# Kernel optimization log

Measured on AMD Instinct MI355X. Metric: run time of the kernel, lower is better.

## Reference

```python
import jax, jax.numpy as jnp
import numpy as np

B, C, W = 32768, 142, 10
K, D = 4096, 128
EPS = 1e-5


def _ln(x, g, b):
    m = jnp.mean(x, axis=-1, keepdims=True)
    v = jnp.var(x, axis=-1, keepdims=True)
    return (x - m) * jax.lax.rsqrt(v + EPS) * g + b


def setup_inputs() -> dict:
    key = jax.random.key(0)
    ks = jax.random.split(key, 10)
    s = lambda fi, fo: (2.0 / (fi + fo)) ** 0.5
    return {
        "x": jax.random.normal(ks[0], (B, C, W), jnp.float32),
        "W1": jax.random.normal(ks[1], (1420, 512), jnp.float32) * s(1420, 512),
        "b1": jnp.zeros((512,), jnp.float32),
        "g1": jnp.ones((512,), jnp.float32),
        "be1": jnp.zeros((512,), jnp.float32),
        "W2": jax.random.normal(ks[2], (512, 256), jnp.float32) * s(512, 256),
        "b2": jnp.zeros((256,), jnp.float32),
        "g2": jnp.ones((256,), jnp.float32),
        "be2": jnp.zeros((256,), jnp.float32),
        "W3": jax.random.normal(ks[3], (256, D), jnp.float32) * s(256, D),
        "b3": jnp.zeros((D,), jnp.float32),
        "emb": jax.random.normal(ks[4], (K, D), jnp.float32),
        "W4": jax.random.normal(ks[5], (D, 256), jnp.float32) * s(D, 256),
        "b4": jnp.zeros((256,), jnp.float32),
        "g3": jnp.ones((256,), jnp.float32),
        "be3": jnp.zeros((256,), jnp.float32),
        "W5": jax.random.normal(ks[6], (256, 128), jnp.float32) * s(256, 128),
        "b5": jnp.zeros((128,), jnp.float32),
        "W6": jax.random.normal(ks[7], (128, 2), jnp.float32) * s(128, 2),
        "b6": jnp.zeros((2,), jnp.float32),
    }


def reference(x, W1, b1, g1, be1, W2, b2, g2, be2, W3, b3, emb,
              W4, b4, g3, be3, W5, b5, W6, b6):
    # ----- encoder (eval mode: dropout is identity) -----
    xf = x.reshape(x.shape[0], -1)                      # [B, 1420]
    h = jax.nn.gelu(_ln(xf @ W1 + b1, g1, be1), approximate=False)
    h = jax.nn.gelu(_ln(h @ W2 + b2, g2, be2), approximate=False)
    z_e = h @ W3 + b3                                   # [B, D]

    # ----- EMA VQ (eval: no buffer updates) -----
    # squared distances give the same argmin as torch.cdist
    d2 = (jnp.sum(z_e * z_e, axis=-1, keepdims=True)
          - 2.0 * (z_e @ emb.T)
          + jnp.sum(emb * emb, axis=-1))                # [B, K]
    indices = jnp.argmin(d2, axis=-1)                   # [B] int
    z_q = emb[indices]                                  # [B, D]

    commitment_loss = 0.25 * jnp.mean((jax.lax.stop_gradient(z_q) - z_e) ** 2)
    z_q_st = z_e + jax.lax.stop_gradient(z_q - z_e)     # straight-through

    # histogram instead of materializing [B, K] one-hot
    counts = jnp.zeros((K,), jnp.float32).at[indices].add(1.0)
    avg_probs = counts / x.shape[0]
    perplexity = jnp.exp(-jnp.sum(avg_probs * jnp.log(avg_probs + 1e-10)))
    n_active = jnp.sum(avg_probs > 0.001)

    # ----- decoder (eval mode) -----
    d = jax.nn.gelu(_ln(z_q_st @ W4 + b4, g3, be3), approximate=False)
    d = jax.nn.gelu(d @ W5 + b5, approximate=False)
    velocity_pred = d @ W6 + b6                         # [B, 2]

    return (velocity_pred, z_e, z_q_st, indices, commitment_loss,
            perplexity, n_active)
```

## Files before the change

kernel.cpp:

```cpp
#include <hip/hip_runtime.h>

#define B_ROWS 32768
#define KCODES 4096

typedef float f32x4 __attribute__((ext_vector_type(4)));
typedef _Float16 f16x8 __attribute__((ext_vector_type(8)));
typedef _Float16 f16x4 __attribute__((ext_vector_type(4)));

struct Split { _Float16 h, m; };

__device__ __forceinline__ Split split2(float v)
{
  Split s;
  s.h = (_Float16)v;
  s.m = (_Float16)((v - (float)s.h) * 256.f);
  return s;
}

template<bool SPLITA>
__global__ __launch_bounds__(256, 3)
void hgemm(const float* __restrict__ Af, const _Float16* __restrict__ Ah,
           const _Float16* __restrict__ Am, int Astr,
           const _Float16* __restrict__ Bh, const _Float16* __restrict__ Bm,
           const float* __restrict__ bias, float* __restrict__ C,
           int M, int N, int K, int Kp, int nbx)
{
  __shared__ _Float16 As1[128 * 40];
  __shared__ _Float16 As2[128 * 40];
  __shared__ _Float16 Bs1[64 * 40];
  __shared__ _Float16 Bs2[64 * 40];

  const int flat = blockIdx.x;
  const int s_   = flat >> 3;
  const int mb   = (s_ / nbx) * 8 + (flat & 7);
  const int nb   = s_ % nbx;
  const int m0   = mb * 128;
  const int n0   = nb * 64;

  const int tid  = threadIdx.x;
  const int lane = tid & 63;
  const int wid  = tid >> 6;
  const int l15  = lane & 15;
  const int lg   = lane >> 4;
  const int wm   = (wid >> 1) * 64;
  const int wn   = (wid & 1) * 32;

  f32x4 hi[4][2], mid[4][2];
  #pragma unroll
  for (int i = 0; i < 4; ++i)
    #pragma unroll
    for (int j = 0; j < 2; ++j) { hi[i][j] = (f32x4)0.f; mid[i][j] = (f32x4)0.f; }

  const int far = tid >> 2;
  const int fak = (tid & 3) << 3;
  const int sar = tid >> 1;
  const int sak = (tid & 1) << 4;
  const int sbn = tid >> 2;
  const int sbk = (tid & 3) << 3;

  float4 va[2][2];
  uint4 ra0, ra1, ra2, ra3;
  uint4 rb0, rb1;

  auto gload = [&](int k0) {
    if (SPLITA) {
      #pragma unroll
      for (int p = 0; p < 2; ++p) {
        const int r = far + (p << 6);
        const int c = k0 + fak;
        const float* src = Af + (size_t)(m0 + r) * K + c;
        va[p][0] = (c < K)     ? *reinterpret_cast<const float4*>(src)
                               : make_float4(0.f, 0.f, 0.f, 0.f);
        va[p][1] = (c + 4 < K) ? *reinterpret_cast<const float4*>(src + 4)
                               : make_float4(0.f, 0.f, 0.f, 0.f);
      }
    } else {
      const size_t gA = (size_t)(m0 + sar) * Astr + k0 + sak;
      ra0 = *reinterpret_cast<const uint4*>(Ah + gA);
      ra1 = *reinterpret_cast<const uint4*>(Ah + gA + 8);
      ra2 = *reinterpret_cast<const uint4*>(Am + gA);
      ra3 = *reinterpret_cast<const uint4*>(Am + gA + 8);
    }
    const size_t gB = (size_t)(n0 + sbn) * Kp + k0 + sbk;
    rb0 = *reinterpret_cast<const uint4*>(Bh + gB);
    rb1 = *reinterpret_cast<const uint4*>(Bm + gB);
  };

  auto lstore = [&]() {
    if (SPLITA) {
      #pragma unroll
      for (int p = 0; p < 2; ++p) {
        const int r = far + (p << 6);
        const Split s0 = split2(va[p][0].x), s1 = split2(va[p][0].y),
                    s2 = split2(va[p][0].z), s3 = split2(va[p][0].w);
        const Split s4 = split2(va[p][1].x), s5 = split2(va[p][1].y),
                    s6 = split2(va[p][1].z), s7 = split2(va[p][1].w);
        f16x8 h, m;
        h[0]=s0.h; h[1]=s1.h; h[2]=s2.h; h[3]=s3.h; h[4]=s4.h; h[5]=s5.h; h[6]=s6.h; h[7]=s7.h;
        m[0]=s0.m; m[1]=s1.m; m[2]=s2.m; m[3]=s3.m; m[4]=s4.m; m[5]=s5.m; m[6]=s6.m; m[7]=s7.m;
        *reinterpret_cast<f16x8*>(&As1[r * 40 + fak]) = h;
        *reinterpret_cast<f16x8*>(&As2[r * 40 + fak]) = m;
      }
    } else {
      const int lA = sar * 40 + sak;
      *reinterpret_cast<uint4*>(&As1[lA])     = ra0;
      *reinterpret_cast<uint4*>(&As1[lA + 8]) = ra1;
      *reinterpret_cast<uint4*>(&As2[lA])     = ra2;
      *reinterpret_cast<uint4*>(&As2[lA + 8]) = ra3;
    }
    const int lB = sbn * 40 + sbk;
    *reinterpret_cast<uint4*>(&Bs1[lB]) = rb0;
    *reinterpret_cast<uint4*>(&Bs2[lB]) = rb1;
  };

  const int nk = Kp >> 5;
  gload(0);
  #pragma unroll 1
  for (int kt = 0; kt < nk; ++kt) {
    lstore();
    __syncthreads();
    if (kt + 1 < nk) gload((kt + 1) << 5);

    f16x8 a1[4], b[2];
    #pragma unroll
    for (int i = 0; i < 4; ++i)
      a1[i] = *reinterpret_cast<const f16x8*>(&As1[(wm + i * 16 + l15) * 40 + 8 * lg]);
    #pragma unroll
    for (int j = 0; j < 2; ++j)
      b[j] = *reinterpret_cast<const f16x8*>(&Bs1[(wn + j * 16 + l15) * 40 + 8 * lg]);
    #pragma unroll
    for (int i = 0; i < 4; ++i)
      #pragma unroll
      for (int j = 0; j < 2; ++j)
        hi[i][j] = __builtin_amdgcn_mfma_f32_16x16x32_f16(a1[i], b[j], hi[i][j], 0, 0, 0);
    #pragma unroll
    for (int i = 0; i < 4; ++i) {
      const f16x8 a2 = *reinterpret_cast<const f16x8*>(&As2[(wm + i * 16 + l15) * 40 + 8 * lg]);
      #pragma unroll
      for (int j = 0; j < 2; ++j)
        mid[i][j] = __builtin_amdgcn_mfma_f32_16x16x32_f16(a2, b[j], mid[i][j], 0, 0, 0);
    }
    #pragma unroll
    for (int j = 0; j < 2; ++j)
      b[j] = *reinterpret_cast<const f16x8*>(&Bs2[(wn + j * 16 + l15) * 40 + 8 * lg]);
    #pragma unroll
    for (int i = 0; i < 4; ++i)
      #pragma unroll
      for (int j = 0; j < 2; ++j)
        mid[i][j] = __builtin_amdgcn_mfma_f32_16x16x32_f16(a1[i], b[j], mid[i][j], 0, 0, 0);
    __syncthreads();
  }

  #pragma unroll
  for (int i = 0; i < 4; ++i)
    #pragma unroll
    for (int j = 0; j < 2; ++j) {
      const int col = n0 + wn + j * 16 + l15;
      const float bs = bias[col];
      #pragma unroll
      for (int r = 0; r < 4; ++r) {
        const int row = m0 + wm + i * 16 + 4 * lg + r;
        C[(size_t)row * N + col] = hi[i][j][r] + 0.00390625f * mid[i][j][r] + bs;
      }
    }
}

__global__ __launch_bounds__(256)
void prep_x(const float* __restrict__ x, _Float16* __restrict__ Xh,
            _Float16* __restrict__ Xm)
{
  const size_t row = blockIdx.x;
  #pragma unroll
  for (int q = 0; q < 6; ++q) {
    const int c = threadIdx.x + 256 * q;
    if (c < 1440) {
      const float v = (c < 1420) ? x[row * 1420 + c] : 0.f;
      const Split s = split2(v);
      Xh[row * 1440 + c] = s.h;
      Xm[row * 1440 + c] = s.m;
    }
  }
}

__global__ __launch_bounds__(256)
void ln_gelu_split(float* __restrict__ buf, const float* __restrict__ g,
                   const float* __restrict__ be, int Wd)
{
  __shared__ float rs[4], rs2[4];
  const int row = blockIdx.x;
  const int tid = threadIdx.x;
  float* x = buf + (size_t)row * Wd;
  const float v0 = x[tid];
  const float v1 = (Wd > 256) ? x[tid + 256] : 0.f;
  float s = v0 + v1, s2 = v0 * v0 + v1 * v1;
  #pragma unroll
  for (int m = 32; m; m >>= 1) { s += __shfl_down(s, m); s2 += __shfl_down(s2, m); }
  const int ln = tid & 63, wv = tid >> 6;
  if (ln == 0) { rs[wv] = s; rs2[wv] = s2; }
  __syncthreads();
  if (tid == 0) {
    const float S = rs[0] + rs[1] + rs[2] + rs[3];
    const float S2 = rs2[0] + rs2[1] + rs2[2] + rs2[3];
    const float mean = S / Wd;
    const float var = S2 / Wd - mean * mean;
    rs[0] = mean; rs2[0] = 1.0f / sqrtf(var + 1e-5f);
  }
  __syncthreads();
  const float mean = rs[0], inv = rs2[0];
  float y0 = (v0 - mean) * inv * g[tid] + be[tid];
  y0 = 0.5f * y0 * (1.f + erff(y0 * 0.70710678118654752f));
  float y1 = 0.f;
  if (Wd > 256) {
    y1 = (v1 - mean) * inv * g[tid + 256] + be[tid + 256];
    y1 = 0.5f * y1 * (1.f + erff(y1 * 0.70710678118654752f));
  }
  _Float16* hb = reinterpret_cast<_Float16*>(x);
  const Split s0 = split2(y0);
  hb[tid] = s0.h; hb[Wd + tid] = s0.m;
  if (Wd > 256) {
    const Split s1 = split2(y1);
    hb[tid + 256] = s1.h; hb[Wd + tid + 256] = s1.m;
  }
}

__global__ __launch_bounds__(256)
void vq_mfma(const float* __restrict__ Z, const _Float16* __restrict__ E1,
             const _Float16* __restrict__ E2, const float* __restrict__ e2,
             float* __restrict__ pval, int* __restrict__ pidx)
{
  __shared__ _Float16 Zs1[64 * 136];
  __shared__ _Float16 Zs2[64 * 136];
  __shared__ _Float16 Es1[128 * 40];
  __shared__ _Float16 Es2[128 * 40];

  const int flat = blockIdx.x;
  const int s_   = flat >> 3;
  const int mb   = (s_ >> 2) * 8 + (flat & 7);
  const int split = s_ & 3;
  const int m0   = mb * 64;

  const int tid  = threadIdx.x;
  const int lane = tid & 63;
  const int wid  = tid >> 6;
  const int l15  = lane & 15;
  const int lg   = lane >> 4;
  const int wn   = wid * 32;

  {
    const int zr = tid >> 2;
    #pragma unroll
    for (int q = 0; q < 8; ++q) {
      const int kk = ((tid & 3) << 2) + (q << 4);
      float4 v = *reinterpret_cast<const float4*>(Z + (size_t)(m0 + zr) * 128 + kk);
      const Split sx = split2(v.x), sy = split2(v.y), sz = split2(v.z), sw = split2(v.w);
      f16x4 h, m;
      h[0] = sx.h; h[1] = sy.h; h[2] = sz.h; h[3] = sw.h;
      m[0] = sx.m; m[1] = sy.m; m[2] = sz.m; m[3] = sw.m;
      *reinterpret_cast<f16x4*>(&Zs1[zr * 136 + kk]) = h;
      *reinterpret_cast<f16x4*>(&Zs2[zr * 136 + kk]) = m;
    }
  }

  float bv[16];
  int   bi[16];
  #pragma unroll
  for (int s = 0; s < 16; ++s) { bv[s] = 3.4e38f; bi[s] = 0x7fffffff; }

  const int sbn = tid >> 1;
  const int sbk = (tid & 1) << 4;
  const int lb  = sbn * 40 + sbk;

  uint4 re0, re1, re2, re3;
  auto eload = [&](int t) {
    const int n0 = split * 1024 + (t >> 2) * 128;
    const int k0 = (t & 3) << 5;
    const size_t gb = (size_t)(n0 + sbn) * 128 + k0 + sbk;
    re0 = *reinterpret_cast<const uint4*>(E1 + gb);
    re1 = *reinterpret_cast<const uint4*>(E1 + gb + 8);
    re2 = *reinterpret_cast<const uint4*>(E2 + gb);
    re3 = *reinterpret_cast<const uint4*>(E2 + gb + 8);
  };

  f32x4 hi[4][2], mid[4][2];

  eload(0);
  #pragma unroll 1
  for (int t = 0; t < 32; ++t) {
    if ((t & 3) == 0) {
      #pragma unroll
      for (int i = 0; i < 4; ++i)
        #pragma unroll
        for (int j = 0; j < 2; ++j) { hi[i][j] = (f32x4)0.f; mid[i][j] = (f32x4)0.f; }
    }
    *reinterpret_cast<uint4*>(&Es1[lb])     = re0;
    *reinterpret_cast<uint4*>(&Es1[lb + 8]) = re1;
    *reinterpret_cast<uint4*>(&Es2[lb])     = re2;
    *reinterpret_cast<uint4*>(&Es2[lb + 8]) = re3;
    __syncthreads();
    if (t + 1 < 32) eload(t + 1);

    const int k0 = (t & 3) << 5;
    f16x8 a1[4], b[2];
    #pragma unroll
    for (int i = 0; i < 4; ++i)
      a1[i] = *reinterpret_cast<const f16x8*>(&Zs1[(i * 16 + l15) * 136 + k0 + 8 * lg]);
    #pragma unroll
    for (int j = 0; j < 2; ++j)
      b[j] = *reinterpret_cast<const f16x8*>(&Es1[(wn + j * 16 + l15) * 40 + 8 * lg]);
    #pragma unroll
    for (int i = 0; i < 4; ++i)
      #pragma unroll
      for (int j = 0; j < 2; ++j)
        hi[i][j] = __builtin_amdgcn_mfma_f32_16x16x32_f16(a1[i], b[j], hi[i][j], 0, 0, 0);
    #pragma unroll
    for (int i = 0; i < 4; ++i) {
      const f16x8 a2 = *reinterpret_cast<const f16x8*>(&Zs2[(i * 16 + l15) * 136 + k0 + 8 * lg]);
      #pragma unroll
      for (int j = 0; j < 2; ++j)
        mid[i][j] = __builtin_amdgcn_mfma_f32_16x16x32_f16(a2, b[j], mid[i][j], 0, 0, 0);
    }
    #pragma unroll
    for (int j = 0; j < 2; ++j)
      b[j] = *reinterpret_cast<const f16x8*>(&Es2[(wn + j * 16 + l15) * 40 + 8 * lg]);
    #pragma unroll
    for (int i = 0; i < 4; ++i)
      #pragma unroll
      for (int j = 0; j < 2; ++j)
        mid[i][j] = __builtin_amdgcn_mfma_f32_16x16x32_f16(a1[i], b[j], mid[i][j], 0, 0, 0);

    if ((t & 3) == 3) {
      const int n0 = split * 1024 + (t >> 2) * 128;
      #pragma unroll
      for (int j = 0; j < 2; ++j) {
        const int c = n0 + wn + j * 16 + l15;
        const float ec = e2[c];
        #pragma unroll
        for (int i = 0; i < 4; ++i)
          #pragma unroll
          for (int r = 0; r < 4; ++r) {
            const float sc = ec - 2.f * (hi[i][j][r] + 0.00390625f * mid[i][j][r]);
            if (sc < bv[i * 4 + r]) { bv[i * 4 + r] = sc; bi[i * 4 + r] = c; }
          }
      }
    }
    __syncthreads();
  }

  #pragma unroll
  for (int s = 0; s < 16; ++s) {
    float v = bv[s]; int ix = bi[s];
    #pragma unroll
    for (int m = 1; m < 16; m <<= 1) {
      const float ov = __shfl_xor(v, m);
      const int   oi = __shfl_xor(ix, m);
      if (ov < v || (ov == v && oi < ix)) { v = ov; ix = oi; }
    }
    if (l15 == 0) {
      const int row = m0 + (s >> 2) * 16 + 4 * lg + (s & 3);
      pval[(size_t)row * 16 + split * 4 + wid] = v;
      pidx[(size_t)row * 16 + split * 4 + wid] = ix;
    }
  }
}

__global__ void prep_wT(const float* __restrict__ W, _Float16* __restrict__ Bh,
                        _Float16* __restrict__ Bm, int K, int N, int nshift,
                        int nmask, int Kp)
{
  const int i = blockIdx.x * 256 + threadIdx.x;
  if (i >= N * Kp) return;
  const int n = i & nmask;
  const int k = i >> nshift;
  const float v = (k < K) ? W[(size_t)k * N + n] : 0.f;
  const Split s = split2(v);
  Bh[(size_t)n * Kp + k] = s.h;
  Bm[(size_t)n * Kp + k] = s.m;
}

__global__ void prep_emb(const float* __restrict__ E, _Float16* __restrict__ E1,
                         _Float16* __restrict__ E2)
{
  const int i = blockIdx.x * 256 + threadIdx.x;
  const Split s = split2(E[i]);
  E1[i] = s.h; E2[i] = s.m;
}

__global__ void vq_reduce(const float* __restrict__ pval, const int* __restrict__ pidx,
                          int* __restrict__ idxout, float* __restrict__ idxf,
                          int* __restrict__ counts)
{
  const int b = blockIdx.x * 256 + threadIdx.x;
  if (b >= B_ROWS) return;
  float best = 3.4e38f; int bix = 0x7fffffff;
  #pragma unroll
  for (int j = 0; j < 16; ++j) {
    const float v = pval[(size_t)b * 16 + j];
    const int   ii = pidx[(size_t)b * 16 + j];
    if (v < best || (v == best && ii < bix)) { best = v; bix = ii; }
  }
  idxout[b] = bix;
  idxf[b] = (float)bix;
  atomicAdd(&counts[bix], 1);
}

__global__ __launch_bounds__(256)
void gather_commit(const int* __restrict__ idx, const float* __restrict__ E,
                   const float* __restrict__ ZE, float* __restrict__ ZQ,
                   float* __restrict__ cpart)
{
  __shared__ float red[4];
  const int b = blockIdx.x * 8 + (threadIdx.x >> 5);
  const int ch = threadIdx.x & 31;
  const int k = idx[b];
  float4 q = *reinterpret_cast<const float4*>(E + (size_t)k * 128 + ch * 4);
  float4 z = *reinterpret_cast<const float4*>(ZE + (size_t)b * 128 + ch * 4);
  *reinterpret_cast<float4*>(ZQ + (size_t)b * 128 + ch * 4) = q;
  float dx = q.x - z.x, dy = q.y - z.y, dz = q.z - z.z, dw = q.w - z.w;
  float s = dx * dx + dy * dy + dz * dz + dw * dw;
  #pragma unroll
  for (int m = 32; m; m >>= 1) s += __shfl_down(s, m);
  const int lane = threadIdx.x & 63, wv = threadIdx.x >> 6;
  if (lane == 0) red[wv] = s;
  __syncthreads();
  if (threadIdx.x == 0) cpart[blockIdx.x] = red[0] + red[1] + red[2] + red[3];
}

__global__ void e2_kernel(const float* __restrict__ E, float* __restrict__ e2)
{
  const int k = blockIdx.x * 256 + threadIdx.x;
  if (k >= KCODES) return;
  float s = 0.f;
  #pragma unroll 4
  for (int d = 0; d < 128; ++d) { float v = E[(size_t)k * 128 + d]; s += v * v; }
  e2[k] = s;
}

__global__ void zero_counts(int* counts)
{
  const int i = blockIdx.x * 256 + threadIdx.x;
  if (i < KCODES) counts[i] = 0;
}

__global__ void gelu_ew(float* __restrict__ p, int n)
{
  const int i = blockIdx.x * 256 + threadIdx.x;
  if (i < n) { float v = p[i]; p[i] = 0.5f * v * (1.f + erff(v * 0.70710678118654752f)); }
}

__global__ void gemm_n2(const float* __restrict__ T, const float* __restrict__ W6,
                        const float* __restrict__ b6, float* __restrict__ V, int M)
{
  const int r = blockIdx.x * 256 + threadIdx.x;
  if (r >= M) return;
  float a0 = b6[0], a1 = b6[1];
  #pragma unroll 4
  for (int d = 0; d < 128; ++d) {
    float t = T[(size_t)r * 128 + d];
    a0 = fmaf(t, W6[d * 2 + 0], a0);
    a1 = fmaf(t, W6[d * 2 + 1], a1);
  }
  V[r * 2 + 0] = a0; V[r * 2 + 1] = a1;
}

__global__ void vel_gather(const int* __restrict__ idx, const float* __restrict__ V,
                           float* __restrict__ out)
{
  const int b = blockIdx.x * 256 + threadIdx.x;
  if (b >= B_ROWS) return;
  const int k = idx[b];
  out[b * 2 + 0] = V[k * 2 + 0];
  out[b * 2 + 1] = V[k * 2 + 1];
}

__global__ __launch_bounds__(256)
void stats_kernel(const float* __restrict__ cpart, const int* __restrict__ counts,
                  float* __restrict__ outs)
{
  __shared__ float sh[256];
  __shared__ float sh2[256];
  __shared__ int shi[256];
  const int t = threadIdx.x;
  float cs = 0.f;
  for (int i = t; i < 4096; i += 256) cs += cpart[i];
  float h = 0.f; int act = 0;
  for (int k = t; k < KCODES; k += 256) {
    float avg = counts[k] * (1.0f / 32768.0f);
    h += avg * logf(avg + 1e-10f);
    act += (avg > 0.001f) ? 1 : 0;
  }
  sh[t] = cs; sh2[t] = h; shi[t] = act;
  __syncthreads();
  for (int s = 128; s; s >>= 1) {
    if (t < s) { sh[t] += sh[t + s]; sh2[t] += sh2[t + s]; shi[t] += shi[t + s]; }
    __syncthreads();
  }
  if (t == 0) {
    outs[0] = 0.25f * sh[0] / (32768.0f * 128.0f);
    outs[1] = expf(-sh2[0]);
    outs[2] = (float)shi[0];
  }
}

extern "C" void kernel_launch(void* const* d_in, const int* in_sizes, int n_in,
                              void* d_out, int out_size, void* d_ws, size_t ws_size,
                              hipStream_t stream)
{
  const float* x   = (const float*)d_in[0];
  const float* W1  = (const float*)d_in[1];
  const float* b1  = (const float*)d_in[2];
  const float* g1  = (const float*)d_in[3];
  const float* be1 = (const float*)d_in[4];
  const float* W2  = (const float*)d_in[5];
  const float* b2  = (const float*)d_in[6];
  const float* g2  = (const float*)d_in[7];
  const float* be2 = (const float*)d_in[8];
  const float* W3  = (const float*)d_in[9];
  const float* b3  = (const float*)d_in[10];
  const float* emb = (const float*)d_in[11];
  const float* W4  = (const float*)d_in[12];
  const float* b4  = (const float*)d_in[13];
  const float* g3  = (const float*)d_in[14];
  const float* be3 = (const float*)d_in[15];
  const float* W5  = (const float*)d_in[16];
  const float* b5  = (const float*)d_in[17];
  const float* W6  = (const float*)d_in[18];
  const float* b6  = (const float*)d_in[19];

  float* out = (float*)d_out;
  float* o_vel  = out;
  float* o_ze   = out + 65536;
  float* o_zq   = out + 65536 + B_ROWS * 128;
  float* o_idx  = out + 65536 + 2 * B_ROWS * 128;
  float* o_scal = o_idx + B_ROWS;

  float* ws = (float*)d_ws;
  float* h1f   = ws;
  float* pval  = ws;
  int*   pidx  = (int*)(ws + 524288);
  float* t1f   = ws + 1048576;
  float* t2    = ws + 2097152;
  float* vv    = ws + 2621440;
  float* h2f   = ws + 16777216;
  float* e2    = ws + 25165824;
  int*   ind   = (int*)(ws + 25169920);
  int*   cnt   = (int*)(ws + 25202688);
  float* cpart = ws + 25206784;
  _Float16* hb  = (_Float16*)(ws + 25210880);
  _Float16* E1  = hb;
  _Float16* E2  = E1 + 524288;
  _Float16* W1a = E2 + 524288;
  _Float16* W1b = W1a + 737280;
  _Float16* W2a = W1b + 737280;
  _Float16* W2b = W2a + 131072;
  _Float16* W3a = W2b + 131072;
  _Float16* W3b = W3a + 32768;
  _Float16* W4a = W3b + 32768;
  _Float16* W4b = W4a + 32768;
  _Float16* W5a = W4b + 32768;
  _Float16* W5b = W5a + 32768;

  _Float16* Xh = (_Float16*)(ws + 26701824);
  _Float16* Xm = Xh + 47185920;
  const bool presplit_x = ws_size >= (size_t)73887744 * 4;

  zero_counts<<<16, 256, 0, stream>>>(cnt);
  e2_kernel<<<16, 256, 0, stream>>>(emb, e2);
  prep_emb<<<2048, 256, 0, stream>>>(emb, E1, E2);
  prep_wT<<<2880, 256, 0, stream>>>(W1, W1a, W1b, 1420, 512, 9, 511, 1440);
  prep_wT<<<512, 256, 0, stream>>>(W2, W2a, W2b, 512, 256, 8, 255, 512);
  prep_wT<<<128, 256, 0, stream>>>(W3, W3a, W3b, 256, 128, 7, 127, 256);
  prep_wT<<<128, 256, 0, stream>>>(W4, W4a, W4b, 128, 256, 8, 255, 128);
  prep_wT<<<128, 256, 0, stream>>>(W5, W5a, W5b, 256, 128, 7, 127, 256);

  if (presplit_x) {
    prep_x<<<B_ROWS, 256, 0, stream>>>(x, Xh, Xm);
    hgemm<false><<<8 * 256, 256, 0, stream>>>(nullptr, Xh, Xm, 1440,
        W1a, W1b, b1, h1f, B_ROWS, 512, 1440, 1440, 8);
  } else {
    hgemm<true><<<8 * 256, 256, 0, stream>>>(x, nullptr, nullptr, 0,
        W1a, W1b, b1, h1f, B_ROWS, 512, 1420, 1440, 8);
  }
  ln_gelu_split<<<B_ROWS, 256, 0, stream>>>(h1f, g1, be1, 512);
  hgemm<false><<<4 * 256, 256, 0, stream>>>(nullptr,
      (const _Float16*)h1f, (const _Float16*)h1f + 512, 1024,
      W2a, W2b, b2, h2f, B_ROWS, 256, 512, 512, 4);
  ln_gelu_split<<<B_ROWS, 256, 0, stream>>>(h2f, g2, be2, 256);
  hgemm<false><<<2 * 256, 256, 0, stream>>>(nullptr,
      (const _Float16*)h2f, (const _Float16*)h2f + 256, 512,
      W3a, W3b, b3, o_ze, B_ROWS, 128, 256, 256, 2);

  vq_mfma<<<2048, 256, 0, stream>>>(o_ze, E1, E2, e2, pval, pidx);
  vq_reduce<<<128, 256, 0, stream>>>(pval, pidx, ind, o_idx, cnt);
  gather_commit<<<4096, 256, 0, stream>>>(ind, emb, o_ze, o_zq, cpart);

  hgemm<false><<<4 * 32, 256, 0, stream>>>(nullptr, E1, E2, 128,
      W4a, W4b, b4, t1f, KCODES, 256, 128, 128, 4);
  ln_gelu_split<<<KCODES, 256, 0, stream>>>(t1f, g3, be3, 256);
  hgemm<false><<<2 * 32, 256, 0, stream>>>(nullptr,
      (const _Float16*)t1f, (const _Float16*)t1f + 256, 512,
      W5a, W5b, b5, t2, KCODES, 128, 256, 256, 2);
  gelu_ew<<<(KCODES * 128 + 255) / 256, 256, 0, stream>>>(t2, KCODES * 128);
  gemm_n2<<<(KCODES + 255) / 256, 256, 0, stream>>>(t2, W6, b6, vv, KCODES);
  vel_gather<<<128, 256, 0, stream>>>(ind, vv, o_vel);

  stats_kernel<<<1, 256, 0, stream>>>(cpart, cnt, o_scal);
}
```

Measured before the change: 849.1 us.

## Prefetch two K-tiles ahead in hgemm and drop x pre-split pass

The hgemm main loop now keeps two register staging sets and issues global loads two K-tiles ahead, so global latency is hidden behind more compute. The separate prep_x kernel that pre-split x into fp16 hi/mid buffers is removed, and layer 1 always splits fp32 x on the fly inside the GEMM. This saves a full extra read and write pass over the large input. The trade-off is more register pressure, extra barriers per iteration, and split arithmetic inside the GEMM loop.

```diff
diff --git a/kernel.cpp b/kernel.cpp
--- a/kernel.cpp
+++ b/kernel.cpp
@@ -58,43 +58,66 @@
   const int sbn = tid >> 2;
   const int sbk = (tid & 3) << 3;
 
-  float4 va[2][2];
-  uint4 ra0, ra1, ra2, ra3;
-  uint4 rb0, rb1;
-
-  auto gload = [&](int k0) {
+  float4 vaA[2][2], vaB[2][2];
+  uint4 raA0, raA1, raA2, raA3, raB0, raB1, raB2, raB3;
+  uint4 rbA0, rbA1, rbB0, rbB1;
+
+  auto gloadA = [&](int k0) {
     if (SPLITA) {
       #pragma unroll
       for (int p = 0; p < 2; ++p) {
         const int r = far + (p << 6);
         const int c = k0 + fak;
         const float* src = Af + (size_t)(m0 + r) * K + c;
-        va[p][0] = (c < K)     ? *reinterpret_cast<const float4*>(src)
-                               : make_float4(0.f, 0.f, 0.f, 0.f);
-        va[p][1] = (c + 4 < K) ? *reinterpret_cast<const float4*>(src + 4)
-                               : make_float4(0.f, 0.f, 0.f, 0.f);
+        vaA[p][0] = (c < K)     ? *reinterpret_cast<const float4*>(src)
+                                : make_float4(0.f, 0.f, 0.f, 0.f);
+        vaA[p][1] = (c + 4 < K) ? *reinterpret_cast<const float4*>(src + 4)
+                                : make_float4(0.f, 0.f, 0.f, 0.f);
       }
     } else {
       const size_t gA = (size_t)(m0 + sar) * Astr + k0 + sak;
-      ra0 = *reinterpret_cast<const uint4*>(Ah + gA);
-      ra1 = *reinterpret_cast<const uint4*>(Ah + gA + 8);
-      ra2 = *reinterpret_cast<const uint4*>(Am + gA);
-      ra3 = *reinterpret_cast<const uint4*>(Am + gA + 8);
+      raA0 = *reinterpret_cast<const uint4*>(Ah + gA);
+      raA1 = *reinterpret_cast<const uint4*>(Ah + gA + 8);
+      raA2 = *reinterpret_cast<const uint4*>(Am + gA);
+      raA3 = *reinterpret_cast<const uint4*>(Am + gA + 8);
     }
     const size_t gB = (size_t)(n0 + sbn) * Kp + k0 + sbk;
-    rb0 = *reinterpret_cast<const uint4*>(Bh + gB);
-    rb1 = *reinterpret_cast<const uint4*>(Bm + gB);
+    rbA0 = *reinterpret_cast<const uint4*>(Bh + gB);
+    rbA1 = *reinterpret_cast<const uint4*>(Bm + gB);
   };
-
-  auto lstore = [&]() {
+  auto gloadB = [&](int k0) {
     if (SPLITA) {
       #pragma unroll
       for (int p = 0; p < 2; ++p) {
         const int r = far + (p << 6);
-        const Split s0 = split2(va[p][0].x), s1 = split2(va[p][0].y),
-                    s2 = split2(va[p][0].z), s3 = split2(va[p][0].w);
-        const Split s4 = split2(va[p][1].x), s5 = split2(va[p][1].y),
-                    s6 = split2(va[p][1].z), s7 = split2(va[p][1].w);
+        const int c = k0 + fak;
+        const float* src = Af + (size_t)(m0 + r) * K + c;
+        vaB[p][0] = (c < K)     ? *reinterpret_cast<const float4*>(src)
+                                : make_float4(0.f, 0.f, 0.f, 0.f);
+        vaB[p][1] = (c + 4 < K) ? *reinterpret_cast<const float4*>(src + 4)
+                                : make_float4(0.f, 0.f, 0.f, 0.f);
+      }
+    } else {
+      const size_t gA = (size_t)(m0 + sar) * Astr + k0 + sak;
+      raB0 = *reinterpret_cast<const uint4*>(Ah + gA);
+      raB1 = *reinterpret_cast<const uint4*>(Ah + gA + 8);
+      raB2 = *reinterpret_cast<const uint4*>(Am + gA);
+      raB3 = *reinterpret_cast<const uint4*>(Am + gA + 8);
+    }
+    const size_t gB = (size_t)(n0 + sbn) * Kp + k0 + sbk;
+    rbB0 = *reinterpret_cast<const uint4*>(Bh + gB);
+    rbB1 = *reinterpret_cast<const uint4*>(Bm + gB);
+  };
+
+  auto lstoreA = [&]() {
+    if (SPLITA) {
+      #pragma unroll
+      for (int p = 0; p < 2; ++p) {
+        const int r = far + (p << 6);
+        const Split s0 = split2(vaA[p][0].x), s1 = split2(vaA[p][0].y),
+                    s2 = split2(vaA[p][0].z), s3 = split2(vaA[p][0].w);
+        const Split s4 = split2(vaA[p][1].x), s5 = split2(vaA[p][1].y),
+                    s6 = split2(vaA[p][1].z), s7 = split2(vaA[p][1].w);
         f16x8 h, m;
         h[0]=s0.h; h[1]=s1.h; h[2]=s2.h; h[3]=s3.h; h[4]=s4.h; h[5]=s5.h; h[6]=s6.h; h[7]=s7.h;
         m[0]=s0.m; m[1]=s1.m; m[2]=s2.m; m[3]=s3.m; m[4]=s4.m; m[5]=s5.m; m[6]=s6.m; m[7]=s7.m;
@@ -103,24 +126,43 @@
       }
     } else {
       const int lA = sar * 40 + sak;
-      *reinterpret_cast<uint4*>(&As1[lA])     = ra0;
-      *reinterpret_cast<uint4*>(&As1[lA + 8]) = ra1;
-      *reinterpret_cast<uint4*>(&As2[lA])     = ra2;
-      *reinterpret_cast<uint4*>(&As2[lA + 8]) = ra3;
+      *reinterpret_cast<uint4*>(&As1[lA])     = raA0;
+      *reinterpret_cast<uint4*>(&As1[lA + 8]) = raA1;
+      *reinterpret_cast<uint4*>(&As2[lA])     = raA2;
+      *reinterpret_cast<uint4*>(&As2[lA + 8]) = raA3;
     }
     const int lB = sbn * 40 + sbk;
-    *reinterpret_cast<uint4*>(&Bs1[lB]) = rb0;
-    *reinterpret_cast<uint4*>(&Bs2[lB]) = rb1;
+    *reinterpret_cast<uint4*>(&Bs1[lB]) = rbA0;
+    *reinterpret_cast<uint4*>(&Bs2[lB]) = rbA1;
   };
-
-  const int nk = Kp >> 5;
-  gload(0);
-  #pragma unroll 1
-  for (int kt = 0; kt < nk; ++kt) {
-    lstore();
-    __syncthreads();
-    if (kt + 1 < nk) gload((kt + 1) << 5);
-
+  auto lstoreB = [&]() {
+    if (SPLITA) {
+      #pragma unroll
+      for (int p = 0; p < 2; ++p) {
+        const int r = far + (p << 6);
+        const Split s0 = split2(vaB[p][0].x), s1 = split2(vaB[p][0].y),
+                    s2 = split2(vaB[p][0].z), s3 = split2(vaB[p][0].w);
+        const Split s4 = split2(vaB[p][1].x), s5 = split2(vaB[p][1].y),
+                    s6 = split2(vaB[p][1].z), s7 = split2(vaB[p][1].w);
+        f16x8 h, m;
+        h[0]=s0.h; h[1]=s1.h; h[2]=s2.h; h[3]=s3.h; h[4]=s4.h; h[5]=s5.h; h[6]=s6.h; h[7]=s7.h;
+        m[0]=s0.m; m[1]=s1.m; m[2]=s2.m; m[3]=s3.m; m[4]=s4.m; m[5]=s5.m; m[6]=s6.m; m[7]=s7.m;
+        *reinterpret_cast<f16x8*>(&As1[r * 40 + fak]) = h;
+        *reinterpret_cast<f16x8*>(&As2[r * 40 + fak]) = m;
+      }
+    } else {
+      const int lA = sar * 40 + sak;
+      *reinterpret_cast<uint4*>(&As1[lA])     = raB0;
+      *reinterpret_cast<uint4*>(&As1[lA + 8]) = raB1;
+      *reinterpret_cast<uint4*>(&As2[lA])     = raB2;
+      *reinterpret_cast<uint4*>(&As2[lA + 8]) = raB3;
+    }
+    const int lB = sbn * 40 + sbk;
+    *reinterpret_cast<uint4*>(&Bs1[lB]) = rbB0;
+    *reinterpret_cast<uint4*>(&Bs2[lB]) = rbB1;
+  };
+
+  auto compute = [&]() {
     f16x8 a1[4], b[2];
     #pragma unroll
     for (int i = 0; i < 4; ++i)
@@ -148,6 +190,30 @@
       #pragma unroll
       for (int j = 0; j < 2; ++j)
         mid[i][j] = __builtin_amdgcn_mfma_f32_16x16x32_f16(a1[i], b[j], mid[i][j], 0, 0, 0);
+  };
+
+  const int nk = Kp >> 5;
+  gloadA(0);
+  gloadB(1 << 5);
+  int kt = 0;
+  #pragma unroll 1
+  while (kt + 2 <= nk) {
+    lstoreA();
+    __syncthreads();
+    if (kt + 2 < nk) gloadA((kt + 2) << 5);
+    compute();
+    __syncthreads();
+    lstoreB();
+    __syncthreads();
+    if (kt + 3 < nk) gloadB((kt + 3) << 5);
+    compute();
+    __syncthreads();
+    kt += 2;
+  }
+  if (kt < nk) {
+    lstoreA();
+    __syncthreads();
+    compute();
     __syncthreads();
   }
 
@@ -163,23 +229,6 @@
         C[(size_t)row * N + col] = hi[i][j][r] + 0.00390625f * mid[i][j][r] + bs;
       }
     }
-}
-
-__global__ __launch_bounds__(256)
-void prep_x(const float* __restrict__ x, _Float16* __restrict__ Xh,
-            _Float16* __restrict__ Xm)
-{
-  const size_t row = blockIdx.x;
-  #pragma unroll
-  for (int q = 0; q < 6; ++q) {
-    const int c = threadIdx.x + 256 * q;
-    if (c < 1440) {
-      const float v = (c < 1420) ? x[row * 1420 + c] : 0.f;
-      const Split s = split2(v);
-      Xh[row * 1440 + c] = s.h;
-      Xm[row * 1440 + c] = s.m;
-    }
-  }
 }
 
 __global__ __launch_bounds__(256)
@@ -559,10 +608,6 @@
   _Float16* W5a = W4b + 32768;
   _Float16* W5b = W5a + 32768;
 
-  _Float16* Xh = (_Float16*)(ws + 26701824);
-  _Float16* Xm = Xh + 47185920;
-  const bool presplit_x = ws_size >= (size_t)73887744 * 4;
-
   zero_counts<<<16, 256, 0, stream>>>(cnt);
   e2_kernel<<<16, 256, 0, stream>>>(emb, e2);
   prep_emb<<<2048, 256, 0, stream>>>(emb, E1, E2);
@@ -572,14 +617,8 @@
   prep_wT<<<128, 256, 0, stream>>>(W4, W4a, W4b, 128, 256, 8, 255, 128);
   prep_wT<<<128, 256, 0, stream>>>(W5, W5a, W5b, 256, 128, 7, 127, 256);
 
-  if (presplit_x) {
-    prep_x<<<B_ROWS, 256, 0, stream>>>(x, Xh, Xm);
-    hgemm<false><<<8 * 256, 256, 0, stream>>>(nullptr, Xh, Xm, 1440,
-        W1a, W1b, b1, h1f, B_ROWS, 512, 1440, 1440, 8);
-  } else {
-    hgemm<true><<<8 * 256, 256, 0, stream>>>(x, nullptr, nullptr, 0,
-        W1a, W1b, b1, h1f, B_ROWS, 512, 1420, 1440, 8);
-  }
+  hgemm<true><<<8 * 256, 256, 0, stream>>>(x, nullptr, nullptr, 0,
+      W1a, W1b, b1, h1f, B_ROWS, 512, 1420, 1440, 8);
   ln_gelu_split<<<B_ROWS, 256, 0, stream>>>(h1f, g1, be1, 512);
   hgemm<false><<<4 * 256, 256, 0, stream>>>(nullptr,
       (const _Float16*)h1f, (const _Float16*)h1f + 512, 1024,
```

After: 974.3 us. 14.7% more time.

## Drop x pre-split pass and fuse decoder GELU into GEMM epilogue

Applied to the files above, without the earlier changes.

Removes the prep_x kernel, which converted x into split fp16 hi/mid buffers in workspace, so the first GEMM always takes the fp32 input and splits it on the fly inside the tile load. It also adds a GELU template flag to the hgemm epilogue and uses it for the W5 decoder GEMM, replacing the separate gelu_ew kernel. The aim is to avoid writing and re-reading a large split copy of x plus one small kernel launch. The cost is extra conversion work inside the W1 GEMM's inner loads, which could slow that GEMM.

```diff
diff --git a/kernel.cpp b/kernel.cpp
--- a/kernel.cpp
+++ b/kernel.cpp
@@ -17,7 +17,12 @@
   return s;
 }
 
-template<bool SPLITA>
+__device__ __forceinline__ float gelu_exact(float v)
+{
+  return 0.5f * v * (1.f + erff(v * 0.70710678118654752f));
+}
+
+template<bool SPLITA, bool GELU>
 __global__ __launch_bounds__(256, 3)
 void hgemm(const float* __restrict__ Af, const _Float16* __restrict__ Ah,
            const _Float16* __restrict__ Am, int Astr,
@@ -160,26 +165,11 @@
       #pragma unroll
       for (int r = 0; r < 4; ++r) {
         const int row = m0 + wm + i * 16 + 4 * lg + r;
-        C[(size_t)row * N + col] = hi[i][j][r] + 0.00390625f * mid[i][j][r] + bs;
+        float v = hi[i][j][r] + 0.00390625f * mid[i][j][r] + bs;
+        if (GELU) v = gelu_exact(v);
+        C[(size_t)row * N + col] = v;
       }
     }
-}
-
-__global__ __launch_bounds__(256)
-void prep_x(const float* __restrict__ x, _Float16* __restrict__ Xh,
-            _Float16* __restrict__ Xm)
-{
-  const size_t row = blockIdx.x;
-  #pragma unroll
-  for (int q = 0; q < 6; ++q) {
-    const int c = threadIdx.x + 256 * q;
-    if (c < 1440) {
-      const float v = (c < 1420) ? x[row * 1420 + c] : 0.f;
-      const Split s = split2(v);
-      Xh[row * 1440 + c] = s.h;
-      Xm[row * 1440 + c] = s.m;
-    }
-  }
 }
 
 __global__ __launch_bounds__(256)
@@ -208,11 +198,11 @@
   __syncthreads();
   const float mean = rs[0], inv = rs2[0];
   float y0 = (v0 - mean) * inv * g[tid] + be[tid];
-  y0 = 0.5f * y0 * (1.f + erff(y0 * 0.70710678118654752f));
+  y0 = gelu_exact(y0);
   float y1 = 0.f;
   if (Wd > 256) {
     y1 = (v1 - mean) * inv * g[tid + 256] + be[tid + 256];
-    y1 = 0.5f * y1 * (1.f + erff(y1 * 0.70710678118654752f));
+    y1 = gelu_exact(y1);
   }
   _Float16* hb = reinterpret_cast<_Float16*>(x);
   const Split s0 = split2(y0);
@@ -439,12 +429,6 @@
 {
   const int i = blockIdx.x * 256 + threadIdx.x;
   if (i < KCODES) counts[i] = 0;
-}
-
-__global__ void gelu_ew(float* __restrict__ p, int n)
-{
-  const int i = blockIdx.x * 256 + threadIdx.x;
-  if (i < n) { float v = p[i]; p[i] = 0.5f * v * (1.f + erff(v * 0.70710678118654752f)); }
 }
 
 __global__ void gemm_n2(const float* __restrict__ T, const float* __restrict__ W6,
@@ -559,10 +543,6 @@
   _Float16* W5a = W4b + 32768;
   _Float16* W5b = W5a + 32768;
 
-  _Float16* Xh = (_Float16*)(ws + 26701824);
-  _Float16* Xm = Xh + 47185920;
-  const bool presplit_x = ws_size >= (size_t)73887744 * 4;
-
   zero_counts<<<16, 256, 0, stream>>>(cnt);
   e2_kernel<<<16, 256, 0, stream>>>(emb, e2);
   prep_emb<<<2048, 256, 0, stream>>>(emb, E1, E2);
@@ -572,20 +552,14 @@
   prep_wT<<<128, 256, 0, stream>>>(W4, W4a, W4b, 128, 256, 8, 255, 128);
   prep_wT<<<128, 256, 0, stream>>>(W5, W5a, W5b, 256, 128, 7, 127, 256);
 
-  if (presplit_x) {
-    prep_x<<<B_ROWS, 256, 0, stream>>>(x, Xh, Xm);
-    hgemm<false><<<8 * 256, 256, 0, stream>>>(nullptr, Xh, Xm, 1440,
-        W1a, W1b, b1, h1f, B_ROWS, 512, 1440, 1440, 8);
-  } else {
-    hgemm<true><<<8 * 256, 256, 0, stream>>>(x, nullptr, nullptr, 0,
-        W1a, W1b, b1, h1f, B_ROWS, 512, 1420, 1440, 8);
-  }
+  hgemm<true, false><<<8 * 256, 256, 0, stream>>>(x, nullptr, nullptr, 0,
+      W1a, W1b, b1, h1f, B_ROWS, 512, 1420, 1440, 8);
   ln_gelu_split<<<B_ROWS, 256, 0, stream>>>(h1f, g1, be1, 512);
-  hgemm<false><<<4 * 256, 256, 0, stream>>>(nullptr,
+  hgemm<false, false><<<4 * 256, 256, 0, stream>>>(nullptr,
       (const _Float16*)h1f, (const _Float16*)h1f + 512, 1024,
       W2a, W2b, b2, h2f, B_ROWS, 256, 512, 512, 4);
   ln_gelu_split<<<B_ROWS, 256, 0, stream>>>(h2f, g2, be2, 256);
-  hgemm<false><<<2 * 256, 256, 0, stream>>>(nullptr,
+  hgemm<false, false><<<2 * 256, 256, 0, stream>>>(nullptr,
       (const _Float16*)h2f, (const _Float16*)h2f + 256, 512,
       W3a, W3b, b3, o_ze, B_ROWS, 128, 256, 256, 2);
 
@@ -593,13 +567,12 @@
   vq_reduce<<<128, 256, 0, stream>>>(pval, pidx, ind, o_idx, cnt);
   gather_commit<<<4096, 256, 0, stream>>>(ind, emb, o_ze, o_zq, cpart);
 
-  hgemm<false><<<4 * 32, 256, 0, stream>>>(nullptr, E1, E2, 128,
+  hgemm<false, false><<<4 * 32, 256, 0, stream>>>(nullptr, E1, E2, 128,
       W4a, W4b, b4, t1f, KCODES, 256, 128, 128, 4);
   ln_gelu_split<<<KCODES, 256, 0, stream>>>(t1f, g3, be3, 256);
-  hgemm<false><<<2 * 32, 256, 0, stream>>>(nullptr,
+  hgemm<false, true><<<2 * 32, 256, 0, stream>>>(nullptr,
       (const _Float16*)t1f, (const _Float16*)t1f + 256, 512,
       W5a, W5b, b5, t2, KCODES, 128, 256, 256, 2);
-  gelu_ew<<<(KCODES * 128 + 255) / 256, 256, 0, stream>>>(t2, KCODES * 128);
   gemm_n2<<<(KCODES + 255) / 256, 256, 0, stream>>>(t2, W6, b6, vv, KCODES);
   vel_gather<<<128, 256, 0, stream>>>(ind, vv, o_vel);
 
```

Result: faster. 799.7 us (-5.8%).
